# Performance work log

Measured on AMD Instinct MI355X. Metric: run time of the kernel, lower is better.

## Reference

```python
import jax, jax.numpy as jnp
import numpy as np

N_NODES, N_EDGES = 50000, 200000
OUT, IN_SELF, EDGE_DIM = 32, 128, 16


def setup_inputs() -> dict:
    key = jax.random.key(0)
    ks = jax.random.split(key, 9)
    return {
        "h_neigh": jax.random.normal(ks[0], (N_NODES, OUT), jnp.float32),
        "h_self": jax.random.normal(ks[1], (N_NODES, IN_SELF), jnp.float32),
        "edge_features": jax.random.normal(ks[2], (N_EDGES, EDGE_DIM), jnp.float32),
        "W_edge": jax.random.normal(ks[3], (OUT * OUT, EDGE_DIM), jnp.float32) * 0.05,
        "b_edge": jax.random.normal(ks[4], (OUT * OUT,), jnp.float32) * 0.05,
        "W_self": jax.random.normal(ks[5], (OUT, IN_SELF), jnp.float32) * 0.05,
        "W_neigh": jax.random.normal(ks[6], (OUT, OUT), jnp.float32) * 0.05,
        "src": jax.random.randint(ks[7], (N_EDGES,), 0, N_NODES),
        "dst": jax.random.randint(ks[8], (N_EDGES,), 0, N_NODES),
    }


def reference(h_neigh, h_self, edge_features, W_edge, b_edge, W_self, W_neigh, src, dst):
    E = edge_features.shape[0]
    N = h_neigh.shape[0]
    out = W_self.shape[0]
    # per-edge weight matrices: [E, out, out]
    ew = (edge_features @ W_edge.T + b_edge).reshape(E, out, out)
    # u_mul_e: m[e,i,j] = h_src[e,j] * ew[e,i,j]; downstream does mean over edges
    # then sum over i. Sum over i commutes with mean, so fuse: s[e,j] =
    # h_src[e,j] * sum_i ew[e,i,j]  -> identical math, [E,out] messages.
    s = h_neigh[src] * ew.sum(axis=1)  # [E, out]
    deg = jax.ops.segment_sum(jnp.ones((E,), s.dtype), dst, num_segments=N)
    agg = jax.ops.segment_sum(s, dst, num_segments=N) / jnp.maximum(deg, 1.0)[:, None]
    z = jax.nn.relu(h_self @ W_self.T + agg @ W_neigh.T)
    return z
```

## Files before the change

kernel.cpp:

```cpp
#include <hip/hip_runtime.h>

#define N_NODES 50000
#define N_EDGES 200000
#define OUT 32
#define IN_SELF 128
#define EDGE_DIM 16

__global__ __launch_bounds__(256) void prep_zero_kernel(
        const float* __restrict__ W_edge, const float* __restrict__ b_edge,
        float* __restrict__ Wcol, float* __restrict__ bcol,
        float4* __restrict__ zero4, int n_zero4) {
    int gid = blockIdx.x * 256 + threadIdx.x;
    for (int i = gid; i < n_zero4; i += gridDim.x * 256) {
        zero4[i] = make_float4(0.f, 0.f, 0.f, 0.f);
    }
    if (blockIdx.x == 0) {
        int t = threadIdx.x;
        for (int i = t; i < OUT * EDGE_DIM; i += 256) {
            int j = i / EDGE_DIM, k = i % EDGE_DIM;
            float s = 0.f;
#pragma unroll
            for (int r = 0; r < OUT; ++r) s += W_edge[(r * OUT + j) * EDGE_DIM + k];
            Wcol[i] = s;
        }
        if (t < OUT) {
            float s = 0.f;
#pragma unroll
            for (int r = 0; r < OUT; ++r) s += b_edge[r * OUT + t];
            bcol[t] = s;
        }
    }
}

__global__ __launch_bounds__(256) void edge_kernel(
        const float* __restrict__ h_neigh, const float* __restrict__ ef,
        const int* __restrict__ src, const int* __restrict__ dst,
        const float* __restrict__ Wcol, const float* __restrict__ bcol,
        float* __restrict__ agg, float* __restrict__ deg, int E) {
    __shared__ float4 wl4[OUT][5];
    __shared__ float4 efl[32][4];
    __shared__ float bl[OUT];
    __shared__ int sdl[32], ddl[32];

    int t = threadIdx.x;
    int e0 = blockIdx.x * 32;
    if (t < 128) {
        wl4[t >> 2][t & 3] = ((const float4*)Wcol)[t];
    } else {
        int i = t - 128;
        int e = e0 + (i >> 2);
        if (e < E) efl[i >> 2][i & 3] = ((const float4*)ef)[(size_t)e * 4 + (i & 3)];
    }
    if (t < 32) {
        bl[t] = bcol[t];
        sdl[t] = (e0 + t < E) ? src[e0 + t] : 0;
    } else if (t < 64) {
        int i = t - 32;
        ddl[i] = (e0 + i < E) ? dst[e0 + i] : 0;
    }
    __syncthreads();

    int g = t >> 5, j = t & 31;
#pragma unroll
    for (int it = 0; it < 4; ++it) {
        int le = g + 8 * it;
        int e = e0 + le;
        if (e >= E) continue;
        int s = sdl[le];
        int d = ddl[le];
        float4 w0 = wl4[j][0], w1 = wl4[j][1], w2 = wl4[j][2], w3 = wl4[j][3];
        float4 f0 = efl[le][0], f1 = efl[le][1], f2 = efl[le][2], f3 = efl[le][3];
        float acc = bl[j];
        acc = fmaf(f0.x, w0.x, acc); acc = fmaf(f0.y, w0.y, acc);
        acc = fmaf(f0.z, w0.z, acc); acc = fmaf(f0.w, w0.w, acc);
        acc = fmaf(f1.x, w1.x, acc); acc = fmaf(f1.y, w1.y, acc);
        acc = fmaf(f1.z, w1.z, acc); acc = fmaf(f1.w, w1.w, acc);
        acc = fmaf(f2.x, w2.x, acc); acc = fmaf(f2.y, w2.y, acc);
        acc = fmaf(f2.z, w2.z, acc); acc = fmaf(f2.w, w2.w, acc);
        acc = fmaf(f3.x, w3.x, acc); acc = fmaf(f3.y, w3.y, acc);
        acc = fmaf(f3.z, w3.z, acc); acc = fmaf(f3.w, w3.w, acc);
        float hv = h_neigh[(size_t)s * OUT + j];
        atomicAdd(&agg[(size_t)d * OUT + j], hv * acc);
        if (j == 0) atomicAdd(&deg[d], 1.0f);
    }
}

__global__ __launch_bounds__(256) void node_kernel(
        const float* __restrict__ h_self, const float* __restrict__ agg,
        const float* __restrict__ deg, const float* __restrict__ W_self,
        const float* __restrict__ W_neigh, float* __restrict__ out, int N) {
    __shared__ float4 ws4[OUT][33];
    __shared__ float4 wn4[OUT][9];
    __shared__ float4 hs4[8][32];
    __shared__ float4 an4[8][8];

    int t = threadIdx.x;
    int n0 = blockIdx.x * 8;

    for (int i = t; i < OUT * (IN_SELF / 4); i += 256)
        ws4[i >> 5][i & 31] = ((const float4*)W_self)[i];
    {
        wn4[t >> 3][t & 7] = ((const float4*)W_neigh)[t];
    }
    {
        int n = n0 + (t >> 5);
        if (n < N) hs4[t >> 5][t & 31] = ((const float4*)h_self)[(size_t)n0 * 32 + t];
    }
    if (t < 64) {
        int ln = t >> 3, k4 = t & 7;
        int n = n0 + ln;
        if (n < N) {
            float r = 1.0f / fmaxf(deg[n], 1.0f);
            float4 v = ((const float4*)agg)[(size_t)n * 8 + k4];
            an4[ln][k4] = make_float4(v.x * r, v.y * r, v.z * r, v.w * r);
        }
    }
    __syncthreads();

    int ln = t >> 5, j = t & 31;
    int n = n0 + ln;
    if (n >= N) return;
    float4 a4 = make_float4(0.f, 0.f, 0.f, 0.f);
#pragma unroll
    for (int k4 = 0; k4 < IN_SELF / 4; ++k4) {
        float4 h = hs4[ln][k4], w = ws4[j][k4];
        a4.x = fmaf(h.x, w.x, a4.x); a4.y = fmaf(h.y, w.y, a4.y);
        a4.z = fmaf(h.z, w.z, a4.z); a4.w = fmaf(h.w, w.w, a4.w);
    }
#pragma unroll
    for (int k4 = 0; k4 < OUT / 4; ++k4) {
        float4 h = an4[ln][k4], w = wn4[j][k4];
        a4.x = fmaf(h.x, w.x, a4.x); a4.y = fmaf(h.y, w.y, a4.y);
        a4.z = fmaf(h.z, w.z, a4.z); a4.w = fmaf(h.w, w.w, a4.w);
    }
    float acc = (a4.x + a4.y) + (a4.z + a4.w);
    out[(size_t)n * OUT + j] = fmaxf(acc, 0.f);
}

extern "C" void kernel_launch(void* const* d_in, const int* in_sizes, int n_in,
                              void* d_out, int out_size, void* d_ws, size_t ws_size,
                              hipStream_t stream) {
    const float* h_neigh = (const float*)d_in[0];
    const float* h_self  = (const float*)d_in[1];
    const float* ef      = (const float*)d_in[2];
    const float* W_edge  = (const float*)d_in[3];
    const float* b_edge  = (const float*)d_in[4];
    const float* W_self  = (const float*)d_in[5];
    const float* W_neigh = (const float*)d_in[6];
    const int*   src     = (const int*)d_in[7];
    const int*   dst     = (const int*)d_in[8];
    float* out = (float*)d_out;

    const int N = N_NODES, E = N_EDGES;

    float* Wcol = (float*)d_ws;
    float* bcol = Wcol + OUT * EDGE_DIM;
    float* deg  = bcol + OUT;
    float* agg  = deg + N;

    const int n_zero4 = (N + N * OUT) / 4;
    const int zgrid = (n_zero4 + 255) / 256;

    prep_zero_kernel<<<zgrid, 256, 0, stream>>>(W_edge, b_edge, Wcol, bcol,
                                                (float4*)deg, n_zero4);

    edge_kernel<<<(E + 31) / 32, 256, 0, stream>>>(h_neigh, ef, src, dst,
                                                   Wcol, bcol, agg, deg, E);

    node_kernel<<<(N + 7) / 8, 256, 0, stream>>>(h_self, agg, deg, W_self,
                                                 W_neigh, out, N);
}
```

Measured before the change: 150.8 us.

## Replace float atomic scatter with per-node linked lists and gather in node kernel

Each edge now writes its message to a per-edge buffer and pushes itself onto a per-destination linked list with one atomicExch. The node kernel walks that list to sum messages and count degree, so the per-feature float atomics and the large zeroing pass are gone. In exchange it adds an E×32 intermediate buffer write and read, plus serial pointer chasing with dependent loads per node. Summation order now depends on list order, which makes results nondeterministic at rounding level.

```diff
diff --git a/kernel.cpp b/kernel.cpp
--- a/kernel.cpp
+++ b/kernel.cpp
@@ -6,14 +6,12 @@
 #define IN_SELF 128
 #define EDGE_DIM 16
 
-__global__ __launch_bounds__(256) void prep_zero_kernel(
+__global__ __launch_bounds__(256) void init_prep_kernel(
         const float* __restrict__ W_edge, const float* __restrict__ b_edge,
         float* __restrict__ Wcol, float* __restrict__ bcol,
-        float4* __restrict__ zero4, int n_zero4) {
+        int* __restrict__ head, int n_head) {
     int gid = blockIdx.x * 256 + threadIdx.x;
-    for (int i = gid; i < n_zero4; i += gridDim.x * 256) {
-        zero4[i] = make_float4(0.f, 0.f, 0.f, 0.f);
-    }
+    for (int i = gid; i < n_head; i += gridDim.x * 256) head[i] = -1;
     if (blockIdx.x == 0) {
         int t = threadIdx.x;
         for (int i = t; i < OUT * EDGE_DIM; i += 256) {
@@ -36,7 +34,8 @@
         const float* __restrict__ h_neigh, const float* __restrict__ ef,
         const int* __restrict__ src, const int* __restrict__ dst,
         const float* __restrict__ Wcol, const float* __restrict__ bcol,
-        float* __restrict__ agg, float* __restrict__ deg, int E) {
+        float* __restrict__ ES, int* __restrict__ head, int* __restrict__ nxt,
+        int E) {
     __shared__ float4 wl4[OUT][5];
     __shared__ float4 efl[32][4];
     __shared__ float bl[OUT];
@@ -80,45 +79,50 @@
         acc = fmaf(f3.x, w3.x, acc); acc = fmaf(f3.y, w3.y, acc);
         acc = fmaf(f3.z, w3.z, acc); acc = fmaf(f3.w, w3.w, acc);
         float hv = h_neigh[(size_t)s * OUT + j];
-        atomicAdd(&agg[(size_t)d * OUT + j], hv * acc);
-        if (j == 0) atomicAdd(&deg[d], 1.0f);
+        ES[(size_t)e * OUT + j] = hv * acc;
+        if (j == 0) {
+            int old = atomicExch(&head[d], e);
+            nxt[e] = old;
+        }
     }
 }
 
 __global__ __launch_bounds__(256) void node_kernel(
-        const float* __restrict__ h_self, const float* __restrict__ agg,
-        const float* __restrict__ deg, const float* __restrict__ W_self,
-        const float* __restrict__ W_neigh, float* __restrict__ out, int N) {
+        const float* __restrict__ h_self, const float* __restrict__ ES,
+        const int* __restrict__ head, const int* __restrict__ nxt,
+        const float* __restrict__ W_self, const float* __restrict__ W_neigh,
+        float* __restrict__ out, int N) {
     __shared__ float4 ws4[OUT][33];
     __shared__ float4 wn4[OUT][9];
     __shared__ float4 hs4[8][32];
-    __shared__ float4 an4[8][8];
+    __shared__ float ans[8][32];
 
     int t = threadIdx.x;
     int n0 = blockIdx.x * 8;
 
     for (int i = t; i < OUT * (IN_SELF / 4); i += 256)
         ws4[i >> 5][i & 31] = ((const float4*)W_self)[i];
-    {
-        wn4[t >> 3][t & 7] = ((const float4*)W_neigh)[t];
-    }
+    wn4[t >> 3][t & 7] = ((const float4*)W_neigh)[t];
     {
         int n = n0 + (t >> 5);
         if (n < N) hs4[t >> 5][t & 31] = ((const float4*)h_self)[(size_t)n0 * 32 + t];
     }
-    if (t < 64) {
-        int ln = t >> 3, k4 = t & 7;
-        int n = n0 + ln;
-        if (n < N) {
-            float r = 1.0f / fmaxf(deg[n], 1.0f);
-            float4 v = ((const float4*)agg)[(size_t)n * 8 + k4];
-            an4[ln][k4] = make_float4(v.x * r, v.y * r, v.z * r, v.w * r);
+
+    int ln = t >> 5, j = t & 31;
+    int n = n0 + ln;
+    if (n < N) {
+        float aggv = 0.f;
+        int cnt = 0;
+        int e = head[n];
+        while (e >= 0) {
+            aggv += ES[(size_t)e * OUT + j];
+            ++cnt;
+            e = nxt[e];
         }
+        ans[ln][j] = aggv / (float)max(cnt, 1);
     }
     __syncthreads();
 
-    int ln = t >> 5, j = t & 31;
-    int n = n0 + ln;
     if (n >= N) return;
     float4 a4 = make_float4(0.f, 0.f, 0.f, 0.f);
 #pragma unroll
@@ -127,9 +131,10 @@
         a4.x = fmaf(h.x, w.x, a4.x); a4.y = fmaf(h.y, w.y, a4.y);
         a4.z = fmaf(h.z, w.z, a4.z); a4.w = fmaf(h.w, w.w, a4.w);
     }
+    const float4* an4 = (const float4*)&ans[ln][0];
 #pragma unroll
     for (int k4 = 0; k4 < OUT / 4; ++k4) {
-        float4 h = an4[ln][k4], w = wn4[j][k4];
+        float4 h = an4[k4], w = wn4[j][k4];
         a4.x = fmaf(h.x, w.x, a4.x); a4.y = fmaf(h.y, w.y, a4.y);
         a4.z = fmaf(h.z, w.z, a4.z); a4.w = fmaf(h.w, w.w, a4.w);
     }
@@ -155,18 +160,15 @@
 
     float* Wcol = (float*)d_ws;
     float* bcol = Wcol + OUT * EDGE_DIM;
-    float* deg  = bcol + OUT;
-    float* agg  = deg + N;
+    int*   head = (int*)(bcol + OUT);
+    int*   nxt  = head + N;
+    float* ES   = (float*)(nxt + E);
 
-    const int n_zero4 = (N + N * OUT) / 4;
-    const int zgrid = (n_zero4 + 255) / 256;
-
-    prep_zero_kernel<<<zgrid, 256, 0, stream>>>(W_edge, b_edge, Wcol, bcol,
-                                                (float4*)deg, n_zero4);
+    init_prep_kernel<<<64, 256, 0, stream>>>(W_edge, b_edge, Wcol, bcol, head, N);
 
     edge_kernel<<<(E + 31) / 32, 256, 0, stream>>>(h_neigh, ef, src, dst,
-                                                   Wcol, bcol, agg, deg, E);
+                                                   Wcol, bcol, ES, head, nxt, E);
 
-    node_kernel<<<(N + 7) / 8, 256, 0, stream>>>(h_self, agg, deg, W_self,
-                                                 W_neigh, out, N);
+    node_kernel<<<(N + 7) / 8, 256, 0, stream>>>(h_self, ES, head, nxt,
+                                                 W_self, W_neigh, out, N);
 }
```

Result: faster. 146.2 us (-3.1%).

## Fuse zero, edge and node stages into one persistent kernel with grid barriers

Applied to the files above, without the earlier changes.

Replaces the zero-fill, edge-scatter and node-transform launches with a single persistent kernel of 1280 blocks. The stages are separated by software grid barriers built on atomic counters, and a tiny prep kernel resets those counters and computes the column sums. This removes launch gaps and per-kernel tail effects. In exchange it relies on all blocks being co-resident and on spin-waiting, and it drops the bounds checks because the sizes divide evenly.

```diff
diff --git a/kernel.cpp b/kernel.cpp
--- a/kernel.cpp
+++ b/kernel.cpp
@@ -6,135 +6,158 @@
 #define IN_SELF 128
 #define EDGE_DIM 16
 
-__global__ __launch_bounds__(256) void prep_zero_kernel(
+#define GRID_P 1280
+#define NCHUNK 6250
+
+struct EdgeSM {
+    float4 wl4[OUT][5];
+    float4 efl[32][4];
+    float  bl[OUT];
+    int    sdl[32], ddl[32];
+};
+struct NodeSM {
+    float4 ws4[OUT][33];
+    float4 wn4[OUT][9];
+    float4 hs4[8][32];
+    float4 an4[8][8];
+};
+union SMU { EdgeSM e; NodeSM n; };
+
+__device__ __forceinline__ void grid_barrier(int* ctr) {
+    __syncthreads();
+    if (threadIdx.x == 0) {
+        __threadfence();
+        atomicAdd(ctr, 1);
+        int polls = 0;
+        while (__hip_atomic_load(ctr, __ATOMIC_RELAXED, __HIP_MEMORY_SCOPE_AGENT)
+                   < GRID_P && polls < 100000000) {
+            __builtin_amdgcn_s_sleep(2);
+            ++polls;
+        }
+    }
+    __syncthreads();
+    __threadfence();
+}
+
+__global__ __launch_bounds__(512) void prep_kernel(
         const float* __restrict__ W_edge, const float* __restrict__ b_edge,
         float* __restrict__ Wcol, float* __restrict__ bcol,
-        float4* __restrict__ zero4, int n_zero4) {
-    int gid = blockIdx.x * 256 + threadIdx.x;
-    for (int i = gid; i < n_zero4; i += gridDim.x * 256) {
-        zero4[i] = make_float4(0.f, 0.f, 0.f, 0.f);
+        int* __restrict__ ctr) {
+    int t = threadIdx.x;
+    if (t < 2) ctr[t] = 0;
+    if (t < OUT * EDGE_DIM) {
+        int j = t / EDGE_DIM, k = t % EDGE_DIM;
+        float s = 0.f;
+#pragma unroll
+        for (int r = 0; r < OUT; ++r) s += W_edge[(r * OUT + j) * EDGE_DIM + k];
+        Wcol[t] = s;
     }
-    if (blockIdx.x == 0) {
-        int t = threadIdx.x;
-        for (int i = t; i < OUT * EDGE_DIM; i += 256) {
-            int j = i / EDGE_DIM, k = i % EDGE_DIM;
-            float s = 0.f;
+    if (t < OUT) {
+        float s = 0.f;
 #pragma unroll
-            for (int r = 0; r < OUT; ++r) s += W_edge[(r * OUT + j) * EDGE_DIM + k];
-            Wcol[i] = s;
-        }
-        if (t < OUT) {
-            float s = 0.f;
-#pragma unroll
-            for (int r = 0; r < OUT; ++r) s += b_edge[r * OUT + t];
-            bcol[t] = s;
-        }
+        for (int r = 0; r < OUT; ++r) s += b_edge[r * OUT + t];
+        bcol[t] = s;
     }
 }
 
-__global__ __launch_bounds__(256) void edge_kernel(
-        const float* __restrict__ h_neigh, const float* __restrict__ ef,
+__global__ __launch_bounds__(256, 6) void fused_kernel(
+        const float* __restrict__ h_neigh, const float* __restrict__ h_self,
+        const float* __restrict__ ef,
         const int* __restrict__ src, const int* __restrict__ dst,
         const float* __restrict__ Wcol, const float* __restrict__ bcol,
-        float* __restrict__ agg, float* __restrict__ deg, int E) {
-    __shared__ float4 wl4[OUT][5];
-    __shared__ float4 efl[32][4];
-    __shared__ float bl[OUT];
-    __shared__ int sdl[32], ddl[32];
+        const float* __restrict__ W_self, const float* __restrict__ W_neigh,
+        float* __restrict__ deg, float* __restrict__ agg,
+        int* __restrict__ ctr, float4* __restrict__ zero4, int n_zero4,
+        float* __restrict__ out) {
+    __shared__ SMU sm;
+    int t = threadIdx.x;
+    int bid = blockIdx.x;
 
-    int t = threadIdx.x;
-    int e0 = blockIdx.x * 32;
-    if (t < 128) {
-        wl4[t >> 2][t & 3] = ((const float4*)Wcol)[t];
-    } else {
-        int i = t - 128;
-        int e = e0 + (i >> 2);
-        if (e < E) efl[i >> 2][i & 3] = ((const float4*)ef)[(size_t)e * 4 + (i & 3)];
-    }
-    if (t < 32) {
-        bl[t] = bcol[t];
-        sdl[t] = (e0 + t < E) ? src[e0 + t] : 0;
-    } else if (t < 64) {
-        int i = t - 32;
-        ddl[i] = (e0 + i < E) ? dst[e0 + i] : 0;
-    }
-    __syncthreads();
+    for (int i = bid * 256 + t; i < n_zero4; i += GRID_P * 256)
+        zero4[i] = make_float4(0.f, 0.f, 0.f, 0.f);
+
+    if (t < 128) sm.e.wl4[t >> 2][t & 3] = ((const float4*)Wcol)[t];
+    if (t < OUT) sm.e.bl[t] = bcol[t];
+
+    grid_barrier(&ctr[0]);
 
     int g = t >> 5, j = t & 31;
+    for (int c = bid; c < NCHUNK; c += GRID_P) {
+        int e0 = c * 32;
+        __syncthreads();
+        if (t < 128) {
+            int e = e0 + (t >> 2);
+            sm.e.efl[t >> 2][t & 3] = ((const float4*)ef)[(size_t)e * 4 + (t & 3)];
+        } else if (t < 160) {
+            sm.e.sdl[t - 128] = src[e0 + t - 128];
+        } else if (t < 192) {
+            sm.e.ddl[t - 160] = dst[e0 + t - 160];
+        }
+        __syncthreads();
 #pragma unroll
-    for (int it = 0; it < 4; ++it) {
-        int le = g + 8 * it;
-        int e = e0 + le;
-        if (e >= E) continue;
-        int s = sdl[le];
-        int d = ddl[le];
-        float4 w0 = wl4[j][0], w1 = wl4[j][1], w2 = wl4[j][2], w3 = wl4[j][3];
-        float4 f0 = efl[le][0], f1 = efl[le][1], f2 = efl[le][2], f3 = efl[le][3];
-        float acc = bl[j];
-        acc = fmaf(f0.x, w0.x, acc); acc = fmaf(f0.y, w0.y, acc);
-        acc = fmaf(f0.z, w0.z, acc); acc = fmaf(f0.w, w0.w, acc);
-        acc = fmaf(f1.x, w1.x, acc); acc = fmaf(f1.y, w1.y, acc);
-        acc = fmaf(f1.z, w1.z, acc); acc = fmaf(f1.w, w1.w, acc);
-        acc = fmaf(f2.x, w2.x, acc); acc = fmaf(f2.y, w2.y, acc);
-        acc = fmaf(f2.z, w2.z, acc); acc = fmaf(f2.w, w2.w, acc);
-        acc = fmaf(f3.x, w3.x, acc); acc = fmaf(f3.y, w3.y, acc);
-        acc = fmaf(f3.z, w3.z, acc); acc = fmaf(f3.w, w3.w, acc);
-        float hv = h_neigh[(size_t)s * OUT + j];
-        atomicAdd(&agg[(size_t)d * OUT + j], hv * acc);
-        if (j == 0) atomicAdd(&deg[d], 1.0f);
+        for (int it = 0; it < 4; ++it) {
+            int le = g + 8 * it;
+            int e = e0 + le;
+            int s = sm.e.sdl[le];
+            int d = sm.e.ddl[le];
+            float4 w0 = sm.e.wl4[j][0], w1 = sm.e.wl4[j][1];
+            float4 w2 = sm.e.wl4[j][2], w3 = sm.e.wl4[j][3];
+            float4 f0 = sm.e.efl[le][0], f1 = sm.e.efl[le][1];
+            float4 f2 = sm.e.efl[le][2], f3 = sm.e.efl[le][3];
+            float acc = sm.e.bl[j];
+            acc = fmaf(f0.x, w0.x, acc); acc = fmaf(f0.y, w0.y, acc);
+            acc = fmaf(f0.z, w0.z, acc); acc = fmaf(f0.w, w0.w, acc);
+            acc = fmaf(f1.x, w1.x, acc); acc = fmaf(f1.y, w1.y, acc);
+            acc = fmaf(f1.z, w1.z, acc); acc = fmaf(f1.w, w1.w, acc);
+            acc = fmaf(f2.x, w2.x, acc); acc = fmaf(f2.y, w2.y, acc);
+            acc = fmaf(f2.z, w2.z, acc); acc = fmaf(f2.w, w2.w, acc);
+            acc = fmaf(f3.x, w3.x, acc); acc = fmaf(f3.y, w3.y, acc);
+            acc = fmaf(f3.z, w3.z, acc); acc = fmaf(f3.w, w3.w, acc);
+            float hv = h_neigh[(size_t)s * OUT + j];
+            atomicAdd(&agg[(size_t)d * OUT + j], hv * acc);
+            if (j == 0) atomicAdd(&deg[d], 1.0f);
+            (void)e;
+        }
     }
-}
 
-__global__ __launch_bounds__(256) void node_kernel(
-        const float* __restrict__ h_self, const float* __restrict__ agg,
-        const float* __restrict__ deg, const float* __restrict__ W_self,
-        const float* __restrict__ W_neigh, float* __restrict__ out, int N) {
-    __shared__ float4 ws4[OUT][33];
-    __shared__ float4 wn4[OUT][9];
-    __shared__ float4 hs4[8][32];
-    __shared__ float4 an4[8][8];
+    grid_barrier(&ctr[1]);
 
-    int t = threadIdx.x;
-    int n0 = blockIdx.x * 8;
+    __syncthreads();
+    for (int i = t; i < OUT * (IN_SELF / 4); i += 256)
+        sm.n.ws4[i >> 5][i & 31] = ((const float4*)W_self)[i];
+    sm.n.wn4[t >> 3][t & 7] = ((const float4*)W_neigh)[t];
 
-    for (int i = t; i < OUT * (IN_SELF / 4); i += 256)
-        ws4[i >> 5][i & 31] = ((const float4*)W_self)[i];
-    {
-        wn4[t >> 3][t & 7] = ((const float4*)W_neigh)[t];
-    }
-    {
-        int n = n0 + (t >> 5);
-        if (n < N) hs4[t >> 5][t & 31] = ((const float4*)h_self)[(size_t)n0 * 32 + t];
-    }
-    if (t < 64) {
-        int ln = t >> 3, k4 = t & 7;
-        int n = n0 + ln;
-        if (n < N) {
+    int ln = t >> 5;
+    for (int c = bid; c < NCHUNK; c += GRID_P) {
+        int n0 = c * 8;
+        __syncthreads();
+        sm.n.hs4[t >> 5][t & 31] = ((const float4*)h_self)[(size_t)n0 * 32 + t];
+        if (t < 64) {
+            int lnn = t >> 3, k4 = t & 7;
+            int n = n0 + lnn;
             float r = 1.0f / fmaxf(deg[n], 1.0f);
             float4 v = ((const float4*)agg)[(size_t)n * 8 + k4];
-            an4[ln][k4] = make_float4(v.x * r, v.y * r, v.z * r, v.w * r);
+            sm.n.an4[lnn][k4] = make_float4(v.x * r, v.y * r, v.z * r, v.w * r);
         }
+        __syncthreads();
+
+        int n = n0 + ln;
+        float4 a4 = make_float4(0.f, 0.f, 0.f, 0.f);
+#pragma unroll
+        for (int k4 = 0; k4 < IN_SELF / 4; ++k4) {
+            float4 h = sm.n.hs4[ln][k4], w = sm.n.ws4[j][k4];
+            a4.x = fmaf(h.x, w.x, a4.x); a4.y = fmaf(h.y, w.y, a4.y);
+            a4.z = fmaf(h.z, w.z, a4.z); a4.w = fmaf(h.w, w.w, a4.w);
+        }
+#pragma unroll
+        for (int k4 = 0; k4 < OUT / 4; ++k4) {
+            float4 h = sm.n.an4[ln][k4], w = sm.n.wn4[j][k4];
+            a4.x = fmaf(h.x, w.x, a4.x); a4.y = fmaf(h.y, w.y, a4.y);
+            a4.z = fmaf(h.z, w.z, a4.z); a4.w = fmaf(h.w, w.w, a4.w);
+        }
+        float acc = (a4.x + a4.y) + (a4.z + a4.w);
+        out[(size_t)n * OUT + j] = fmaxf(acc, 0.f);
     }
-    __syncthreads();
-
-    int ln = t >> 5, j = t & 31;
-    int n = n0 + ln;
-    if (n >= N) return;
-    float4 a4 = make_float4(0.f, 0.f, 0.f, 0.f);
-#pragma unroll
-    for (int k4 = 0; k4 < IN_SELF / 4; ++k4) {
-        float4 h = hs4[ln][k4], w = ws4[j][k4];
-        a4.x = fmaf(h.x, w.x, a4.x); a4.y = fmaf(h.y, w.y, a4.y);
-        a4.z = fmaf(h.z, w.z, a4.z); a4.w = fmaf(h.w, w.w, a4.w);
-    }
-#pragma unroll
-    for (int k4 = 0; k4 < OUT / 4; ++k4) {
-        float4 h = an4[ln][k4], w = wn4[j][k4];
-        a4.x = fmaf(h.x, w.x, a4.x); a4.y = fmaf(h.y, w.y, a4.y);
-        a4.z = fmaf(h.z, w.z, a4.z); a4.w = fmaf(h.w, w.w, a4.w);
-    }
-    float acc = (a4.x + a4.y) + (a4.z + a4.w);
-    out[(size_t)n * OUT + j] = fmaxf(acc, 0.f);
 }
 
 extern "C" void kernel_launch(void* const* d_in, const int* in_sizes, int n_in,
@@ -151,22 +174,20 @@
     const int*   dst     = (const int*)d_in[8];
     float* out = (float*)d_out;
 
-    const int N = N_NODES, E = N_EDGES;
+    const int N = N_NODES;
 
     float* Wcol = (float*)d_ws;
     float* bcol = Wcol + OUT * EDGE_DIM;
-    float* deg  = bcol + OUT;
+    int*   ctr  = (int*)(bcol + OUT);
+    float* deg  = (float*)d_ws + 560;
     float* agg  = deg + N;
 
     const int n_zero4 = (N + N * OUT) / 4;
-    const int zgrid = (n_zero4 + 255) / 256;
 
-    prep_zero_kernel<<<zgrid, 256, 0, stream>>>(W_edge, b_edge, Wcol, bcol,
-                                                (float4*)deg, n_zero4);
+    prep_kernel<<<1, 512, 0, stream>>>(W_edge, b_edge, Wcol, bcol, ctr);
 
-    edge_kernel<<<(E + 31) / 32, 256, 0, stream>>>(h_neigh, ef, src, dst,
-                                                   Wcol, bcol, agg, deg, E);
-
-    node_kernel<<<(N + 7) / 8, 256, 0, stream>>>(h_self, agg, deg, W_self,
-                                                 W_neigh, out, N);
+    fused_kernel<<<GRID_P, 256, 0, stream>>>(h_neigh, h_self, ef, src, dst,
+                                             Wcol, bcol, W_self, W_neigh,
+                                             deg, agg, ctr,
+                                             (float4*)deg, n_zero4, out);
 }
```

Result: slower. 493.5 us (+227.2%).
